# Performance work log

Measured on AMD Instinct MI355X. Metric: run time of the kernel, lower is better.

The kernel has to match this reference:

```python
import jax, jax.numpy as jnp
import numpy as np
from jax import lax

BN_EPS = 1e-5

def dwconv(x, w, dilation):
    # x: [N,C,H,W], w: [C,1,k,k] depthwise; SAME padding = (r*(k-1)+1)//2
    k = w.shape[-1]
    pad = (dilation * (k - 1) + 1) // 2
    return lax.conv_general_dilated(
        x, w, window_strides=(1, 1), padding=[(pad, pad), (pad, pad)],
        rhs_dilation=(dilation, dilation), feature_group_count=x.shape[1],
        dimension_numbers=('NCHW', 'OIHW', 'NCHW'))

def bn_eval(y, gamma, beta, mean, var):
    # inference BatchNorm2d over channel dim; params: [C]
    inv = gamma * lax.rsqrt(var + BN_EPS)
    return y * inv[None, :, None, None] + (beta - mean * inv)[None, :, None, None]

def setup_inputs() -> dict:
    key = jax.random.key(0)
    ks = jax.random.split(key, 13)
    C = 384
    x = jax.random.normal(ks[0], (16, C, 56, 56), jnp.float32)
    w_lk = jax.random.normal(ks[1], (C, 1, 13, 13), jnp.float32) * 0.05
    w_b0 = jax.random.normal(ks[2], (C, 1, 5, 5), jnp.float32) * 0.05
    w_b1 = jax.random.normal(ks[3], (C, 1, 7, 7), jnp.float32) * 0.05
    w_b2 = jax.random.normal(ks[4], (C, 1, 7, 7), jnp.float32) * 0.05
    w_b3 = jax.random.normal(ks[5], (C, 1, 3, 3), jnp.float32) * 0.05
    w_b4 = jax.random.normal(ks[6], (C, 1, 3, 3), jnp.float32) * 0.05
    w_b5 = jax.random.normal(ks[7], (C, 1, 3, 3), jnp.float32) * 0.05
    bn_gamma = jax.random.uniform(ks[8], (7, C), jnp.float32, 0.5, 1.5)
    bn_beta = jax.random.normal(ks[9], (7, C), jnp.float32) * 0.1
    bn_mean = jax.random.normal(ks[10], (7, C), jnp.float32) * 0.1
    bn_var = jax.random.uniform(ks[11], (7, C), jnp.float32, 0.5, 1.5)
    return dict(x=x, w_lk=w_lk, w_b0=w_b0, w_b1=w_b1, w_b2=w_b2, w_b3=w_b3,
                w_b4=w_b4, w_b5=w_b5, bn_gamma=bn_gamma, bn_beta=bn_beta,
                bn_mean=bn_mean, bn_var=bn_var)

def reference(x, w_lk, w_b0, w_b1, w_b2, w_b3, w_b4, w_b5,
              bn_gamma, bn_beta, bn_mean, bn_var):
    # DilatedReparamBlock (kernel_size=13, non-deploy):
    # out = BN(dw13(x)) + sum_i BN_i(dw_{k_i, r_i}(x))
    dilates = (1, 1, 2, 3, 4, 5)
    branch_ws = (w_b0, w_b1, w_b2, w_b3, w_b4, w_b5)
    out = bn_eval(dwconv(x, w_lk, 1), bn_gamma[0], bn_beta[0], bn_mean[0], bn_var[0])
    for i, (w, r) in enumerate(zip(branch_ws, dilates)):
        j = i + 1
        out = out + bn_eval(dwconv(x, w, r), bn_gamma[j], bn_beta[j], bn_mean[j], bn_var[j])
    return out
```

## Files before the change

### kernel.cpp

```cpp
#include <hip/hip_runtime.h>


#define CCH 384
#define SP 56
#define PW 68
#define NPLANES (16*384)

__global__ __launch_bounds__(64) void drb_conv13_w64(
    const float* __restrict__ x,
    const float* __restrict__ w_lk, const float* __restrict__ w_b0,
    const float* __restrict__ w_b1, const float* __restrict__ w_b2,
    const float* __restrict__ w_b3, const float* __restrict__ w_b4,
    const float* __restrict__ w_b5,
    const float* __restrict__ gamma, const float* __restrict__ beta,
    const float* __restrict__ mean, const float* __restrict__ var,
    float* __restrict__ out)
{
    __shared__ __align__(16) float sx[PW * PW];
    __shared__ __align__(16) float sw[13 * 16];

    const int plane = blockIdx.x;
    const int c = plane % CCH;
    const int tid = threadIdx.x;
    const float* __restrict__ xp = x + (size_t)plane * (SP * SP);

    float S[7];
    float bias = 0.f;
    #pragma unroll
    for (int j = 0; j < 7; j++) {
        float inv = gamma[j * CCH + c] * rsqrtf(var[j * CCH + c] + 1e-5f);
        S[j] = inv;
        bias += beta[j * CCH + c] - mean[j * CCH + c] * inv;
    }

    {
        float4 z = make_float4(0.f, 0.f, 0.f, 0.f);
        #pragma unroll
        for (int k = 0; k < 19; k++) {
            int i = tid + 64 * k;
            if (i < PW * PW / 4) ((float4*)sx)[i] = z;
        }
    }

    #pragma unroll
    for (int k = 0; k < 4; k++) {
        int t = tid + 64 * k;
        if (t < 13 * 16) {
            int ky = t >> 4, kx = t & 15;
            float w = 0.f;
            if (kx < 13) {
                w = S[0] * w_lk[c * 169 + ky * 13 + kx];
                if (ky >= 4 && ky <= 8 && kx >= 4 && kx <= 8)
                    w += S[1] * w_b0[c * 25 + (ky - 4) * 5 + (kx - 4)];
                if (ky >= 3 && ky <= 9 && kx >= 3 && kx <= 9)
                    w += S[2] * w_b1[c * 49 + (ky - 3) * 7 + (kx - 3)];
                if (!(ky & 1) && !(kx & 1))
                    w += S[3] * w_b2[c * 49 + (ky >> 1) * 7 + (kx >> 1)];
                if (ky >= 3 && ky <= 9 && (ky - 3) % 3 == 0 &&
                    kx >= 3 && kx <= 9 && (kx - 3) % 3 == 0)
                    w += S[4] * w_b3[c * 9 + ((ky - 3) / 3) * 3 + (kx - 3) / 3];
                if (ky >= 2 && ky <= 10 && (ky - 2) % 4 == 0 &&
                    kx >= 2 && kx <= 10 && (kx - 2) % 4 == 0)
                    w += S[5] * w_b4[c * 9 + ((ky - 2) / 4) * 3 + (kx - 2) / 4];
                if (ky >= 1 && ky <= 11 && (ky - 1) % 5 == 0 &&
                    kx >= 1 && kx <= 11 && (kx - 1) % 5 == 0)
                    w += S[6] * w_b5[c * 9 + ((ky - 1) / 5) * 3 + (kx - 1) / 5];
            }
            sw[t] = w;
        }
    }

    #pragma unroll
    for (int k = 0; k < 13; k++) {
        int i4 = tid + 64 * k;
        if (i4 < SP * SP / 4) {
            float4 v = ((const float4*)xp)[i4];
            int r = i4 / 14;
            int col = (i4 - r * 14) * 4;
            float* d = &sx[(r + 6) * PW + col + 6];
            ((float2*)d)[0] = make_float2(v.x, v.y);
            ((float2*)d)[1] = make_float2(v.z, v.w);
        }
    }
    __syncthreads();

    const int xg = tid & 7;
    const int yg = tid >> 3;
    const int xgc = (xg < 7) ? xg : 3;
    const int Yb = yg * 7;
    const float* __restrict__ sbase = &sx[Yb * PW + 8 * xgc];

    float acc[7][8];
    #pragma unroll
    for (int r = 0; r < 7; r++)
        #pragma unroll
        for (int j = 0; j < 8; j++) acc[r][j] = 0.f;

    #pragma unroll 1
    for (int k0 = 0; k0 < 12; k0 += 2) {
        float4 w0[4], w1[4];
        #pragma unroll
        for (int q = 0; q < 4; q++) {
            w0[q] = ((const float4*)&sw[k0 * 16])[q];
            w1[q] = ((const float4*)&sw[(k0 + 1) * 16])[q];
        }
        const float* sr = sbase + k0 * PW;
        #pragma unroll
        for (int i = 0; i < 8; i++) {
            float4 win4[5];
            #pragma unroll
            for (int q = 0; q < 5; q++)
                win4[q] = *(const float4*)(sr + i * PW + 4 * q);
            const float* win = (const float*)win4;
            if (i < 7) {
                #pragma unroll
                for (int kx = 0; kx < 13; kx++) {
                    const float wv = ((const float*)w0)[kx];
                    #pragma unroll
                    for (int j = 0; j < 8; j++)
                        acc[i][j] = fmaf(wv, win[kx + j], acc[i][j]);
                }
            }
            if (i >= 1) {
                #pragma unroll
                for (int kx = 0; kx < 13; kx++) {
                    const float wv = ((const float*)w1)[kx];
                    #pragma unroll
                    for (int j = 0; j < 8; j++)
                        acc[i - 1][j] = fmaf(wv, win[kx + j], acc[i - 1][j]);
                }
            }
        }
    }
    {
        float4 wt[4];
        #pragma unroll
        for (int q = 0; q < 4; q++) wt[q] = ((const float4*)&sw[12 * 16])[q];
        const float* sr = sbase + 12 * PW;
        #pragma unroll
        for (int i = 0; i < 7; i++) {
            float4 win4[5];
            #pragma unroll
            for (int q = 0; q < 5; q++)
                win4[q] = *(const float4*)(sr + i * PW + 4 * q);
            const float* win = (const float*)win4;
            #pragma unroll
            for (int kx = 0; kx < 13; kx++) {
                const float wv = ((const float*)wt)[kx];
                #pragma unroll
                for (int j = 0; j < 8; j++)
                    acc[i][j] = fmaf(wv, win[kx + j], acc[i][j]);
            }
        }
    }

    if (xg < 7) {
        float* op = out + (size_t)plane * (SP * SP) + Yb * SP + 8 * xg;
        #pragma unroll
        for (int r = 0; r < 7; r++) {
            float4 v0 = make_float4(acc[r][0] + bias, acc[r][1] + bias,
                                    acc[r][2] + bias, acc[r][3] + bias);
            float4 v1 = make_float4(acc[r][4] + bias, acc[r][5] + bias,
                                    acc[r][6] + bias, acc[r][7] + bias);
            *(float4*)(op + r * SP) = v0;
            *(float4*)(op + r * SP + 4) = v1;
        }
    }
}

extern "C" void kernel_launch(void* const* d_in, const int* in_sizes, int n_in,
                              void* d_out, int out_size, void* d_ws, size_t ws_size,
                              hipStream_t stream) {
    const float* x    = (const float*)d_in[0];
    const float* w_lk = (const float*)d_in[1];
    const float* w_b0 = (const float*)d_in[2];
    const float* w_b1 = (const float*)d_in[3];
    const float* w_b2 = (const float*)d_in[4];
    const float* w_b3 = (const float*)d_in[5];
    const float* w_b4 = (const float*)d_in[6];
    const float* w_b5 = (const float*)d_in[7];
    const float* bn_g = (const float*)d_in[8];
    const float* bn_b = (const float*)d_in[9];
    const float* bn_m = (const float*)d_in[10];
    const float* bn_v = (const float*)d_in[11];
    float* out = (float*)d_out;

    drb_conv13_w64<<<dim3(NPLANES), dim3(64), 0, stream>>>(
        x, w_lk, w_b0, w_b1, w_b2, w_b3, w_b4, w_b5,
        bn_g, bn_b, bn_m, bn_v, out);
}
```

Measured before the change: 245.9 us.

## Use 128-thread blocks with 4-wide output tiles and scalarized weights

Doubles the threads per plane to 128, so each thread computes a 7x4 output tile instead of 7x8. It processes four kernel rows per pass, loading the weights into SGPRs via readfirstlane so they become scalar operands. It also adds a sync between zeroing shared memory and filling it. The aim is more parallelism and lower VGPR pressure, at the cost of more redundant shared-memory window loads per output (16 floats for 4 outputs versus 20 for 8) and a wave where 2 of 16 lanes per row do redundant work.

Measured after the change: 258.5 us. 5.1% more time.

```diff
diff --git a/kernel.cpp b/kernel.cpp
--- a/kernel.cpp
+++ b/kernel.cpp
@@ -6,7 +6,11 @@
 #define PW 68
 #define NPLANES (16*384)
 
-__global__ __launch_bounds__(64) void drb_conv13_w64(
+__device__ __forceinline__ float rfl(float v) {
+    return __int_as_float(__builtin_amdgcn_readfirstlane(__float_as_int(v)));
+}
+
+__global__ __launch_bounds__(128, 4) void drb_conv13_w128(
     const float* __restrict__ x,
     const float* __restrict__ w_lk, const float* __restrict__ w_b0,
     const float* __restrict__ w_b1, const float* __restrict__ w_b2,
@@ -36,15 +40,16 @@
     {
         float4 z = make_float4(0.f, 0.f, 0.f, 0.f);
         #pragma unroll
-        for (int k = 0; k < 19; k++) {
-            int i = tid + 64 * k;
+        for (int k = 0; k < 10; k++) {
+            int i = tid + 128 * k;
             if (i < PW * PW / 4) ((float4*)sx)[i] = z;
         }
     }
-
-    #pragma unroll
-    for (int k = 0; k < 4; k++) {
-        int t = tid + 64 * k;
+    __syncthreads();
+
+    #pragma unroll
+    for (int k = 0; k < 2; k++) {
+        int t = tid + 128 * k;
         if (t < 13 * 16) {
             int ky = t >> 4, kx = t & 15;
             float w = 0.f;
@@ -71,8 +76,8 @@
     }
 
     #pragma unroll
-    for (int k = 0; k < 13; k++) {
-        int i4 = tid + 64 * k;
+    for (int k = 0; k < 7; k++) {
+        int i4 = tid + 128 * k;
         if (i4 < SP * SP / 4) {
             float4 v = ((const float4*)xp)[i4];
             int r = i4 / 14;
@@ -84,86 +89,94 @@
     }
     __syncthreads();
 
-    const int xg = tid & 7;
-    const int yg = tid >> 3;
-    const int xgc = (xg < 7) ? xg : 3;
+    const int xg = tid & 15;
+    const int yg = tid >> 4;
+    const int xgc = (xg < 14) ? xg : (xg - 8);
     const int Yb = yg * 7;
-    const float* __restrict__ sbase = &sx[Yb * PW + 8 * xgc];
-
-    float acc[7][8];
+    const float* __restrict__ sbase = &sx[Yb * PW + 4 * xgc];
+
+    float acc[7][4];
     #pragma unroll
     for (int r = 0; r < 7; r++)
         #pragma unroll
-        for (int j = 0; j < 8; j++) acc[r][j] = 0.f;
+        for (int j = 0; j < 4; j++) acc[r][j] = 0.f;
 
     #pragma unroll 1
-    for (int k0 = 0; k0 < 12; k0 += 2) {
-        float4 w0[4], w1[4];
-        #pragma unroll
-        for (int q = 0; q < 4; q++) {
-            w0[q] = ((const float4*)&sw[k0 * 16])[q];
-            w1[q] = ((const float4*)&sw[(k0 + 1) * 16])[q];
+    for (int k0 = 0; k0 < 12; k0 += 4) {
+        float w[4][13];
+        #pragma unroll
+        for (int dy = 0; dy < 4; dy++) {
+            const float* wr = &sw[(k0 + dy) * 16];
+            float4 a = ((const float4*)wr)[0];
+            float4 b = ((const float4*)wr)[1];
+            float4 cq = ((const float4*)wr)[2];
+            float dl = wr[12];
+            w[dy][0] = rfl(a.x);  w[dy][1] = rfl(a.y);
+            w[dy][2] = rfl(a.z);  w[dy][3] = rfl(a.w);
+            w[dy][4] = rfl(b.x);  w[dy][5] = rfl(b.y);
+            w[dy][6] = rfl(b.z);  w[dy][7] = rfl(b.w);
+            w[dy][8] = rfl(cq.x); w[dy][9] = rfl(cq.y);
+            w[dy][10] = rfl(cq.z); w[dy][11] = rfl(cq.w);
+            w[dy][12] = rfl(dl);
         }
         const float* sr = sbase + k0 * PW;
         #pragma unroll
-        for (int i = 0; i < 8; i++) {
-            float4 win4[5];
-            #pragma unroll
-            for (int q = 0; q < 5; q++)
+        for (int i = 0; i < 10; i++) {
+            float4 win4[4];
+            #pragma unroll
+            for (int q = 0; q < 4; q++)
                 win4[q] = *(const float4*)(sr + i * PW + 4 * q);
             const float* win = (const float*)win4;
-            if (i < 7) {
-                #pragma unroll
-                for (int kx = 0; kx < 13; kx++) {
-                    const float wv = ((const float*)w0)[kx];
+            #pragma unroll
+            for (int dy = 0; dy < 4; dy++) {
+                const int r = i - dy;
+                if (r >= 0 && r < 7) {
                     #pragma unroll
-                    for (int j = 0; j < 8; j++)
-                        acc[i][j] = fmaf(wv, win[kx + j], acc[i][j]);
+                    for (int kx = 0; kx < 13; kx++) {
+                        const float wv = w[dy][kx];
+                        #pragma unroll
+                        for (int j = 0; j < 4; j++)
+                            acc[r][j] = fmaf(wv, win[kx + j], acc[r][j]);
+                    }
                 }
             }
-            if (i >= 1) {
-                #pragma unroll
-                for (int kx = 0; kx < 13; kx++) {
-                    const float wv = ((const float*)w1)[kx];
-                    #pragma unroll
-                    for (int j = 0; j < 8; j++)
-                        acc[i - 1][j] = fmaf(wv, win[kx + j], acc[i - 1][j]);
-                }
-            }
         }
     }
     {
-        float4 wt[4];
-        #pragma unroll
-        for (int q = 0; q < 4; q++) wt[q] = ((const float4*)&sw[12 * 16])[q];
+        float w12[13];
+        const float* wr = &sw[12 * 16];
+        float4 a = ((const float4*)wr)[0];
+        float4 b = ((const float4*)wr)[1];
+        float4 cq = ((const float4*)wr)[2];
+        float dl = wr[12];
+        w12[0] = rfl(a.x);  w12[1] = rfl(a.y);  w12[2] = rfl(a.z);  w12[3] = rfl(a.w);
+        w12[4] = rfl(b.x);  w12[5] = rfl(b.y);  w12[6] = rfl(b.z);  w12[7] = rfl(b.w);
+        w12[8] = rfl(cq.x); w12[9] = rfl(cq.y); w12[10] = rfl(cq.z); w12[11] = rfl(cq.w);
+        w12[12] = rfl(dl);
         const float* sr = sbase + 12 * PW;
         #pragma unroll
         for (int i = 0; i < 7; i++) {
-            float4 win4[5];
-            #pragma unroll
-            for (int q = 0; q < 5; q++)
+            float4 win4[4];
+            #pragma unroll
+            for (int q = 0; q < 4; q++)
                 win4[q] = *(const float4*)(sr + i * PW + 4 * q);
             const float* win = (const float*)win4;
             #pragma unroll
             for (int kx = 0; kx < 13; kx++) {
-                const float wv = ((const float*)wt)[kx];
+                const float wv = w12[kx];
                 #pragma unroll
-                for (int j = 0; j < 8; j++)
+                for (int j = 0; j < 4; j++)
                     acc[i][j] = fmaf(wv, win[kx + j], acc[i][j]);
             }
         }
     }
 
-    if (xg < 7) {
-        float* op = out + (size_t)plane * (SP * SP) + Yb * SP + 8 * xg;
+    if (xg < 14) {
+        float* op = out + (size_t)plane * (SP * SP) + Yb * SP + 4 * xg;
         #pragma unroll
         for (int r = 0; r < 7; r++) {
-            float4 v0 = make_float4(acc[r][0] + bias, acc[r][1] + bias,
-                                    acc[r][2] + bias, acc[r][3] + bias);
-            float4 v1 = make_float4(acc[r][4] + bias, acc[r][5] + bias,
-                                    acc[r][6] + bias, acc[r][7] + bias);
-            *(float4*)(op + r * SP) = v0;
-            *(float4*)(op + r * SP + 4) = v1;
+            *(float4*)(op + r * SP) = make_float4(acc[r][0] + bias, acc[r][1] + bias,
+                                                  acc[r][2] + bias, acc[r][3] + bias);
         }
     }
 }
@@ -185,7 +198,7 @@
     const float* bn_v = (const float*)d_in[11];
     float* out = (float*)d_out;
 
-    drb_conv13_w64<<<dim3(NPLANES), dim3(64), 0, stream>>>(
+    drb_conv13_w128<<<dim3(NPLANES), dim3(128), 0, stream>>>(
         x, w_lk, w_b0, w_b1, w_b2, w_b3, w_b4, w_b5,
         bn_g, bn_b, bn_m, bn_v, out);
 }
```

## Use scalar weights via readfirstlane, 4-row vertical blocking, early global prefetch

Applied to the files above, without the earlier changes.

Each weight is broadcast into a scalar register with readfirstlane, which frees vector registers and lets the FMAs take an SGPR operand. The vertical loop now processes four kernel rows per pass, so each loaded input window row is reused across four accumulator rows and LDS traffic drops. Global input loads are issued into registers at kernel start, before the BN and weight setup, to overlap memory latency. Launch bounds now request two blocks per CU. The 13 staged float4 values plus the larger unroll raise register pressure and risk spills.

Result: faster. 227.1 us (-7.6%).

```diff
diff --git a/kernel.cpp b/kernel.cpp
--- a/kernel.cpp
+++ b/kernel.cpp
@@ -6,7 +6,11 @@
 #define PW 68
 #define NPLANES (16*384)
 
-__global__ __launch_bounds__(64) void drb_conv13_w64(
+__device__ __forceinline__ float rfl(float v) {
+    return __int_as_float(__builtin_amdgcn_readfirstlane(__float_as_int(v)));
+}
+
+__global__ __launch_bounds__(64, 2) void drb_conv13_r7(
     const float* __restrict__ x,
     const float* __restrict__ w_lk, const float* __restrict__ w_b0,
     const float* __restrict__ w_b1, const float* __restrict__ w_b2,
@@ -23,6 +27,13 @@
     const int c = plane % CCH;
     const int tid = threadIdx.x;
     const float* __restrict__ xp = x + (size_t)plane * (SP * SP);
+
+    float4 stage[13];
+    #pragma unroll
+    for (int k = 0; k < 13; k++) {
+        int i4 = tid + 64 * k;
+        if (i4 < SP * SP / 4) stage[k] = ((const float4*)xp)[i4];
+    }
 
     float S[7];
     float bias = 0.f;
@@ -74,12 +85,11 @@
     for (int k = 0; k < 13; k++) {
         int i4 = tid + 64 * k;
         if (i4 < SP * SP / 4) {
-            float4 v = ((const float4*)xp)[i4];
             int r = i4 / 14;
             int col = (i4 - r * 14) * 4;
             float* d = &sx[(r + 6) * PW + col + 6];
-            ((float2*)d)[0] = make_float2(v.x, v.y);
-            ((float2*)d)[1] = make_float2(v.z, v.w);
+            ((float2*)d)[0] = make_float2(stage[k].x, stage[k].y);
+            ((float2*)d)[1] = make_float2(stage[k].z, stage[k].w);
         }
     }
     __syncthreads();
@@ -97,45 +107,52 @@
         for (int j = 0; j < 8; j++) acc[r][j] = 0.f;
 
     #pragma unroll 1
-    for (int k0 = 0; k0 < 12; k0 += 2) {
-        float4 w0[4], w1[4];
-        #pragma unroll
-        for (int q = 0; q < 4; q++) {
-            w0[q] = ((const float4*)&sw[k0 * 16])[q];
-            w1[q] = ((const float4*)&sw[(k0 + 1) * 16])[q];
+    for (int k0 = 0; k0 < 12; k0 += 4) {
+        float w[4][13];
+        #pragma unroll
+        for (int dy = 0; dy < 4; dy++) {
+            const float* wr = &sw[(k0 + dy) * 16];
+            #pragma unroll
+            for (int q = 0; q < 3; q++) {
+                float4 t = ((const float4*)wr)[q];
+                w[dy][4*q+0] = rfl(t.x); w[dy][4*q+1] = rfl(t.y);
+                w[dy][4*q+2] = rfl(t.z); w[dy][4*q+3] = rfl(t.w);
+            }
+            w[dy][12] = rfl(wr[12]);
         }
         const float* sr = sbase + k0 * PW;
         #pragma unroll
-        for (int i = 0; i < 8; i++) {
+        for (int i = 0; i < 10; i++) {
             float4 win4[5];
             #pragma unroll
             for (int q = 0; q < 5; q++)
                 win4[q] = *(const float4*)(sr + i * PW + 4 * q);
             const float* win = (const float*)win4;
-            if (i < 7) {
-                #pragma unroll
-                for (int kx = 0; kx < 13; kx++) {
-                    const float wv = ((const float*)w0)[kx];
+            #pragma unroll
+            for (int dy = 0; dy < 4; dy++) {
+                const int r = i - dy;
+                if (r >= 0 && r < 7) {
                     #pragma unroll
-                    for (int j = 0; j < 8; j++)
-                        acc[i][j] = fmaf(wv, win[kx + j], acc[i][j]);
+                    for (int kx = 0; kx < 13; kx++) {
+                        const float wv = w[dy][kx];
+                        #pragma unroll
+                        for (int j = 0; j < 8; j++)
+                            acc[r][j] = fmaf(wv, win[kx + j], acc[r][j]);
+                    }
                 }
             }
-            if (i >= 1) {
-                #pragma unroll
-                for (int kx = 0; kx < 13; kx++) {
-                    const float wv = ((const float*)w1)[kx];
-                    #pragma unroll
-                    for (int j = 0; j < 8; j++)
-                        acc[i - 1][j] = fmaf(wv, win[kx + j], acc[i - 1][j]);
-                }
-            }
         }
     }
     {
-        float4 wt[4];
-        #pragma unroll
-        for (int q = 0; q < 4; q++) wt[q] = ((const float4*)&sw[12 * 16])[q];
+        float w12[13];
+        const float* wr = &sw[12 * 16];
+        #pragma unroll
+        for (int q = 0; q < 3; q++) {
+            float4 t = ((const float4*)wr)[q];
+            w12[4*q+0] = rfl(t.x); w12[4*q+1] = rfl(t.y);
+            w12[4*q+2] = rfl(t.z); w12[4*q+3] = rfl(t.w);
+        }
+        w12[12] = rfl(wr[12]);
         const float* sr = sbase + 12 * PW;
         #pragma unroll
         for (int i = 0; i < 7; i++) {
@@ -146,7 +163,7 @@
             const float* win = (const float*)win4;
             #pragma unroll
             for (int kx = 0; kx < 13; kx++) {
-                const float wv = ((const float*)wt)[kx];
+                const float wv = w12[kx];
                 #pragma unroll
                 for (int j = 0; j < 8; j++)
                     acc[i][j] = fmaf(wv, win[kx + j], acc[i][j]);
@@ -185,7 +202,7 @@
     const float* bn_v = (const float*)d_in[11];
     float* out = (float*)d_out;
 
-    drb_conv13_w64<<<dim3(NPLANES), dim3(64), 0, stream>>>(
+    drb_conv13_r7<<<dim3(NPLANES), dim3(64), 0, stream>>>(
         x, w_lk, w_b0, w_b1, w_b2, w_b3, w_b4, w_b5,
         bn_g, bn_b, bn_m, bn_v, out);
 }
```
